# Optimization experiments

Measured on AMD Instinct MI355X. Metric: run time of the kernel, lower is better.

The kernel has to match this reference:

```python
import jax, jax.numpy as jnp
import numpy as np

EPS = 1e-5  # torch BatchNorm1d default eps
N_NODES, N_EDGES, F_IN, HID, N_LAYERS = 100000, 1600000, 128, 128, 3


def batchnorm(x):
    # affine=False, track_running_stats=False -> normalize with batch stats (biased var)
    m = x.mean(axis=0)
    v = x.var(axis=0)
    return (x - m) / jnp.sqrt(v + EPS)


def gcn_conv(x, W, b, src, dst, deg_inv_sqrt, n):
    # PyG GCNConv: add self-loops, symmetric norm D^-1/2 (A+I) D^-1/2, then linear.
    h = x @ W  # [N, H]
    norm = deg_inv_sqrt[src] * deg_inv_sqrt[dst]  # [E]
    agg = jax.ops.segment_sum(h[src] * norm[:, None], dst, num_segments=n)
    agg = agg + h * (deg_inv_sqrt ** 2)[:, None]  # self-loop term (norm = 1/deg_i)
    return agg + b


def setup_inputs() -> dict:
    key = jax.random.key(0)
    ks = jax.random.split(key, 12)
    x = jax.random.normal(ks[0], (N_NODES, F_IN), dtype=jnp.float32)
    edge_index = jax.random.randint(ks[1], (2, N_EDGES), 0, N_NODES, dtype=jnp.int32)
    s = 1.0 / np.sqrt(F_IN)
    W0 = jax.random.uniform(ks[2], (F_IN, HID), jnp.float32, -s, s)
    b0 = jax.random.uniform(ks[3], (HID,), jnp.float32, -s, s)
    sh = 1.0 / np.sqrt(HID)
    Ws = jax.random.uniform(ks[4], (N_LAYERS - 1, HID, HID), jnp.float32, -sh, sh)
    bs = jax.random.uniform(ks[5], (N_LAYERS - 1, HID), jnp.float32, -sh, sh)
    lin1_w = jax.random.uniform(ks[6], (HID, HID), jnp.float32, -sh, sh)
    lin1_b = jax.random.uniform(ks[7], (HID,), jnp.float32, -sh, sh)
    lin2_w = jax.random.uniform(ks[8], (HID, 2), jnp.float32, -sh, sh)
    lin2_b = jax.random.uniform(ks[9], (2,), jnp.float32, -sh, sh)
    return {"x": x, "edge_index": edge_index, "W0": W0, "b0": b0, "Ws": Ws,
            "bs": bs, "lin1_w": lin1_w, "lin1_b": lin1_b, "lin2_w": lin2_w, "lin2_b": lin2_b}


def reference(x, edge_index, W0, b0, Ws, bs, lin1_w, lin1_b, lin2_w, lin2_b):
    n = x.shape[0]
    src, dst = edge_index[0], edge_index[1]
    # degree with self-loops (computed on target nodes, as in PyG)
    deg = jax.ops.segment_sum(jnp.ones_like(dst, dtype=x.dtype), dst, num_segments=n) + 1.0
    deg_inv_sqrt = deg ** -0.5
    x = jax.nn.relu(batchnorm(gcn_conv(x, W0, b0, src, dst, deg_inv_sqrt, n)))
    for i in range(Ws.shape[0]):
        x = jax.nn.relu(batchnorm(gcn_conv(x, Ws[i], bs[i], src, dst, deg_inv_sqrt, n)))
    x = jax.nn.relu(batchnorm(x @ lin1_w + lin1_b))
    return x @ lin2_w + lin2_b
```

## Files before the change

kernel.cpp:

```cpp
#include <hip/hip_runtime.h>
#include <hip/hip_fp16.h>
#include <math.h>

#define HID 128
#define EPS 1e-5f
#define NBUCK 256
#define BCAP 10240
#define TILE 8192

typedef _Float16 half8 __attribute__((ext_vector_type(8)));
typedef _Float16 half4v __attribute__((ext_vector_type(4)));
typedef float f32x4 __attribute__((ext_vector_type(4)));

__global__ __launch_bounds__(256) void setup(float* __restrict__ psums,
                                             const float* __restrict__ W0,
                                             const float* __restrict__ Ws,
                                             const float* __restrict__ lin1w,
                                             _Float16* __restrict__ Wht,
                                             int* __restrict__ bcur,
                                             _Float16* __restrict__ zrow) {
    int g = blockIdx.x * 256 + threadIdx.x;
    if (g < 4 * 65536) psums[g] = 0.f;
    if (g < 65536) {
        int m = g >> 14;
        int idx = g & 16383;
        int n = idx >> 7, k = idx & 127;
        const float* W = (m == 0) ? W0 : (m == 1) ? Ws : (m == 2) ? (Ws + 16384) : lin1w;
        Wht[(size_t)m * 16384 + n * 128 + k] = (_Float16)W[k * 128 + n];
    }
    if (g < NBUCK) bcur[g] = 0;
    if (g < 128) zrow[g] = (_Float16)0.f;
}

__global__ __launch_bounds__(512) void bin_edges(const int* __restrict__ src, const int* __restrict__ dst,
                                                 int* __restrict__ bcur, int* __restrict__ pairPack, int E) {
    __shared__ int lpack[TILE];
    __shared__ unsigned char lbuck[TILE];
    __shared__ int hist[NBUCK], hscan[NBUCK], cur[NBUCK], delta[NBUCK];
    const int t = threadIdx.x;
    const int base = blockIdx.x * TILE;

    if (t < NBUCK) hist[t] = 0;
    __syncthreads();

    int pk[16], bk[16];
#pragma unroll
    for (int i = 0; i < 16; ++i) {
        int e = base + t + 512 * i;
        if (e < E) {
            int s = src[e], d = dst[e];
            pk[i] = (s << 9) | (d & 511);
            bk[i] = d >> 9;
            atomicAdd(&hist[bk[i]], 1);
        } else {
            bk[i] = -1;
        }
    }
    __syncthreads();

    int v = (t < NBUCK) ? hist[t] : 0;
    if (t < NBUCK) hscan[t] = v;
    __syncthreads();
    for (int off = 1; off < NBUCK; off <<= 1) {
        int u = (t >= off && t < NBUCK) ? hscan[t - off] : 0;
        __syncthreads();
        if (t < NBUCK) hscan[t] += u;
        __syncthreads();
    }
    if (t < NBUCK) cur[t] = hscan[t] - v;
    __syncthreads();

#pragma unroll
    for (int i = 0; i < 16; ++i) {
        if (bk[i] >= 0) {
            int p = atomicAdd(&cur[bk[i]], 1);
            lpack[p] = pk[i];
            lbuck[p] = (unsigned char)bk[i];
        }
    }
    __syncthreads();

    if (t < NBUCK) {
        int c = hist[t];
        if (c > 0) {
            int gbase = t * BCAP + atomicAdd(&bcur[t], c);
            delta[t] = gbase - (hscan[t] - c);
        }
    }
    __syncthreads();

    int total = hscan[NBUCK - 1];
    for (int i = t; i < total; i += 512) {
        int b = lbuck[i];
        pairPack[delta[b] + i] = lpack[i];
    }
}

__global__ __launch_bounds__(512) void bucket_csr(const int* __restrict__ pairPack,
                                                  const int* __restrict__ bcur,
                                                  int* __restrict__ cnt, float* __restrict__ dis,
                                                  int* __restrict__ rowptr,
                                                  int* __restrict__ srcsort, int N) {
    __shared__ int spair[BCAP];
    __shared__ int deg[512], sc[512], cur[512];
    const int b = blockIdx.x;
    const int t = threadIdx.x;
    deg[t] = 0;
    __syncthreads();
    int n = bcur[b];
    if (n > BCAP) n = BCAP;
    const int base = b * BCAP;
    for (int i = t; i < n; i += 512) {
        int p = pairPack[base + i];
        spair[i] = p;
        atomicAdd(&deg[p & 511], 1);
    }
    __syncthreads();
    int node = b * 512 + t;
    int d = deg[t];
    sc[t] = d;
    __syncthreads();
    for (int off = 1; off < 512; off <<= 1) {
        int u = (t >= off) ? sc[t - off] : 0;
        __syncthreads();
        sc[t] += u;
        __syncthreads();
    }
    int myoff = sc[t] - d;
    cur[t] = myoff;
    if (node < N) {
        cnt[node] = d;
        dis[node] = rsqrtf((float)d + 1.0f);
        rowptr[node] = base + myoff;
    }
    __syncthreads();
    for (int i = t; i < n; i += 512) {
        int p = spair[i];
        int pos = atomicAdd(&cur[p & 511], 1);
        srcsort[base + pos] = p >> 9;
    }
}

template <bool INF16, bool NORM, bool SCALEOUT, bool STATS>
__global__ __launch_bounds__(512) void gemm_mfma(const float* __restrict__ Xf,
                                                 const _Float16* __restrict__ Xh,
                                                 const _Float16* __restrict__ Wht,
                                                 const float* __restrict__ mean, const float* __restrict__ rstd,
                                                 const float* __restrict__ dis,
                                                 _Float16* __restrict__ Yh,
                                                 float* __restrict__ psum, float* __restrict__ psumsq,
                                                 int N) {
    __shared__ _Float16 sX[128 * 136];
    __shared__ _Float16 sW[128 * 136];
    __shared__ float gsum[STATS ? 8 : 1][128], gsq[STATS ? 8 : 1][128];
    const int tid = threadIdx.x;
    const int r0 = blockIdx.x * 128;

#pragma unroll
    for (int i = 0; i < 4; ++i) {
        int f = tid + 512 * i;
        int n = f >> 4;
        int k8 = (f & 15) * 8;
        *(half8*)&sW[n * 136 + k8] = *(const half8*)&Wht[n * 128 + k8];
    }

    if (INF16) {
#pragma unroll
        for (int i = 0; i < 4; ++i) {
            int f = tid + 512 * i;
            int rr = f >> 4;
            int c8 = (f & 15) * 8;
            int gr = r0 + rr;
            half8 hv = (half8)(_Float16)0.f;
            if (gr < N) hv = *(const half8*)&Xh[(size_t)gr * 128 + c8];
            if (NORM) {
#pragma unroll
                for (int e = 0; e < 8; ++e) {
                    float u = ((float)hv[e] - mean[c8 + e]) * rstd[c8 + e];
                    hv[e] = (_Float16)fmaxf(u, 0.f);
                }
            }
            *(half8*)&sX[rr * 136 + c8] = hv;
        }
    } else {
#pragma unroll
        for (int i = 0; i < 8; ++i) {
            int f = tid + 512 * i;
            int rr = f >> 5;
            int c4 = (f & 31) * 4;
            int gr = r0 + rr;
            float4 v = make_float4(0.f, 0.f, 0.f, 0.f);
            if (gr < N) v = *(const float4*)&Xf[(size_t)gr * 128 + c4];
            if (NORM) {
                float4 m4 = *(const float4*)&mean[c4];
                float4 s4 = *(const float4*)&rstd[c4];
                v.x = fmaxf((v.x - m4.x) * s4.x, 0.f);
                v.y = fmaxf((v.y - m4.y) * s4.y, 0.f);
                v.z = fmaxf((v.z - m4.z) * s4.z, 0.f);
                v.w = fmaxf((v.w - m4.w) * s4.w, 0.f);
            }
            half4v h;
            h.x = (_Float16)v.x; h.y = (_Float16)v.y; h.z = (_Float16)v.z; h.w = (_Float16)v.w;
            *(half4v*)&sX[rr * 136 + c4] = h;
        }
    }
    __syncthreads();

    const int wv = tid >> 6;
    const int lane = tid & 63;
    const int ln = lane & 15;
    const int quad = lane >> 4;

    half8 a[4];
    {
        const _Float16* sA = &sX[(wv * 16 + ln) * 136 + quad * 8];
#pragma unroll
        for (int kc = 0; kc < 4; ++kc) a[kc] = *(const half8*)&sA[kc * 32];
    }

    f32x4 acc[8];
#pragma unroll
    for (int ct = 0; ct < 8; ++ct) acc[ct] = (f32x4){0.f, 0.f, 0.f, 0.f};

    const _Float16* wbase = &sW[ln * 136 + quad * 8];
#pragma unroll
    for (int kc = 0; kc < 4; ++kc) {
#pragma unroll
        for (int ct = 0; ct < 8; ++ct) {
            half8 b = *(const half8*)&wbase[ct * 16 * 136 + kc * 32];
            acc[ct] = __builtin_amdgcn_mfma_f32_16x16x32_f16(a[kc], b, acc[ct], 0, 0, 0);
        }
    }

    float dv[4];
    int rr[4];
#pragma unroll
    for (int rg = 0; rg < 4; ++rg) {
        rr[rg] = r0 + wv * 16 + quad * 4 + rg;
        dv[rg] = (SCALEOUT && rr[rg] < N) ? dis[rr[rg]] : 1.f;
    }

    __syncthreads();
#pragma unroll
    for (int ct = 0; ct < 8; ++ct) {
        int col = ct * 16 + ln;
#pragma unroll
        for (int rg = 0; rg < 4; ++rg)
            sX[(wv * 16 + quad * 4 + rg) * 136 + col] = (_Float16)(acc[ct][rg] * dv[rg]);
    }
    __syncthreads();
#pragma unroll
    for (int i = 0; i < 4; ++i) {
        int f = tid + 512 * i;
        int rrr = f >> 4;
        int c8 = (f & 15) * 8;
        int gr = r0 + rrr;
        if (gr < N) *(half8*)&Yh[(size_t)gr * 128 + c8] = *(const half8*)&sX[rrr * 136 + c8];
    }

    if (STATS) {
#pragma unroll
        for (int ct = 0; ct < 8; ++ct) {
            float s = 0.f, s2 = 0.f;
#pragma unroll
            for (int rg = 0; rg < 4; ++rg) {
                if (rr[rg] < N) {
                    float v = acc[ct][rg];
                    s += v;
                    s2 += v * v;
                }
            }
            s += __shfl_xor(s, 16, 64);
            s += __shfl_xor(s, 32, 64);
            s2 += __shfl_xor(s2, 16, 64);
            s2 += __shfl_xor(s2, 32, 64);
            if (quad == 0) {
                gsum[wv][ct * 16 + ln] = s;
                gsq[wv][ct * 16 + ln] = s2;
            }
        }
        __syncthreads();
        int bkt = (blockIdx.x & 7) * 128;
        if (tid < 128) {
            float s = 0.f;
#pragma unroll
            for (int i = 0; i < 8; ++i) s += gsum[i][tid];
            atomicAdd(&psum[bkt + tid], s);
        } else if (tid < 256) {
            int c = tid - 128;
            float s2 = 0.f;
#pragma unroll
            for (int i = 0; i < 8; ++i) s2 += gsq[i][c];
            atomicAdd(&psumsq[bkt + c], s2);
        }
    }
}

__global__ __launch_bounds__(256) void aggregate_f16(const __half* __restrict__ hs,
                                                     const float* __restrict__ dis,
                                                     const int* __restrict__ rowptr,
                                                     const int* __restrict__ cnt,
                                                     const int* __restrict__ srcsort,
                                                     __half* __restrict__ outP,
                                                     float* __restrict__ psum, float* __restrict__ psumsq,
                                                     int N) {
    __shared__ float asum[4][128], asq[4][128];
    const int wv = threadIdx.x >> 6;
    const int lane = threadIdx.x & 63;
    const __half2* h2 = (const __half2*)hs;
    __half2* out2 = (__half2*)outP;
    const __half2 z = __float2half2_rn(0.f);

    float sx = 0.f, sy = 0.f, qx = 0.f, qy = 0.f;

#pragma unroll
    for (int rep = 0; rep < 4; ++rep) {
        const int node = __builtin_amdgcn_readfirstlane(blockIdx.x * 16 + wv * 4 + rep);

        __half2 acch[4];
        acch[0] = h2[(size_t)node * 64 + lane];
        acch[1] = z; acch[2] = z; acch[3] = z;

        const int beg = rowptr[node];
        const int end = beg + cnt[node];
        int e = beg;
        for (; e + 16 <= end; e += 16) {
            int s[16];
#pragma unroll
            for (int j = 0; j < 16; ++j) s[j] = srcsort[e + j];
            __half2 v[16];
#pragma unroll
            for (int j = 0; j < 16; ++j) v[j] = h2[(size_t)s[j] * 64 + lane];
#pragma unroll
            for (int j = 0; j < 16; ++j) acch[j & 3] = __hadd2(acch[j & 3], v[j]);
        }
        for (; e + 4 <= end; e += 4) {
            int s[4];
#pragma unroll
            for (int j = 0; j < 4; ++j) s[j] = srcsort[e + j];
            __half2 v[4];
#pragma unroll
            for (int j = 0; j < 4; ++j) v[j] = h2[(size_t)s[j] * 64 + lane];
#pragma unroll
            for (int j = 0; j < 4; ++j) acch[j & 3] = __hadd2(acch[j & 3], v[j]);
        }
        for (; e < end; ++e) {
            acch[0] = __hadd2(acch[0], h2[(size_t)srcsort[e] * 64 + lane]);
        }

        float2 f0 = __half22float2(acch[0]);
        float2 f1 = __half22float2(acch[1]);
        float2 f2 = __half22float2(acch[2]);
        float2 f3 = __half22float2(acch[3]);
        float di = dis[node];
        float rx = ((f0.x + f1.x) + (f2.x + f3.x)) * di;
        float ry = ((f0.y + f1.y) + (f2.y + f3.y)) * di;
        out2[(size_t)node * 64 + lane] = __floats2half2_rn(rx, ry);
        sx += rx; sy += ry;
        qx += rx * rx; qy += ry * ry;
    }

    asum[wv][2 * lane] = sx;
    asum[wv][2 * lane + 1] = sy;
    asq[wv][2 * lane] = qx;
    asq[wv][2 * lane + 1] = qy;
    __syncthreads();
    const int t = threadIdx.x;
    int bkt = (blockIdx.x & 255) * 128;
    if (t < 128) {
        float s = asum[0][t] + asum[1][t] + asum[2][t] + asum[3][t];
        atomicAdd(&psum[bkt + t], s);
    } else {
        int c = t - 128;
        float s2 = asq[0][c] + asq[1][c] + asq[2][c] + asq[3][c];
        atomicAdd(&psumsq[bkt + c], s2);
    }
}

__global__ __launch_bounds__(256) void finalize_stats_par(const float* __restrict__ psum,
                                                          const float* __restrict__ psumsq,
                                                          float* __restrict__ meanf, float* __restrict__ rstdf,
                                                          int N) {
    __shared__ float ls[256], ls2[256];
    int c = blockIdx.x;
    int t = threadIdx.x;
    ls[t] = psum[t * 128 + c];
    ls2[t] = psumsq[t * 128 + c];
    __syncthreads();
    for (int off = 128; off >= 1; off >>= 1) {
        if (t < off) { ls[t] += ls[t + off]; ls2[t] += ls2[t + off]; }
        __syncthreads();
    }
    if (t == 0) {
        float m = ls[0] / (float)N;
        float var = ls2[0] / (float)N - m * m;
        meanf[c] = m;
        rstdf[c] = rsqrtf(var + EPS);
    }
}

__global__ __launch_bounds__(256) void lin2_kernel(const __half* __restrict__ Q,
                                                   const float* __restrict__ psum,
                                                   const float* __restrict__ psumsq,
                                                   const float* __restrict__ W2,
                                                   const float* __restrict__ b2, float* __restrict__ out, int N) {
    __shared__ float sw0[128], sw1[128], sm[128], srs[128];
    int t = threadIdx.x;
    if (t < 128) {
        float s = 0.f, s2 = 0.f;
#pragma unroll
        for (int b = 0; b < 8; ++b) {
            s += psum[b * 128 + t];
            s2 += psumsq[b * 128 + t];
        }
        float m = s / (float)N;
        sm[t] = m;
        srs[t] = rsqrtf(s2 / (float)N - m * m + EPS);
        sw0[t] = W2[2 * t];
        sw1[t] = W2[2 * t + 1];
    }
    __syncthreads();
    int r = blockIdx.x * 256 + t;
    if (r >= N) return;
    const __half2* q2 = (const __half2*)Q;
    float acc0 = b2[0], acc1 = b2[1];
#pragma unroll 8
    for (int k2 = 0; k2 < 64; ++k2) {
        float2 f = __half22float2(q2[(size_t)r * 64 + k2]);
        int k = 2 * k2;
        float v0 = fmaxf((f.x - sm[k]) * srs[k], 0.f);
        float v1 = fmaxf((f.y - sm[k + 1]) * srs[k + 1], 0.f);
        acc0 += v0 * sw0[k] + v1 * sw0[k + 1];
        acc1 += v0 * sw1[k] + v1 * sw1[k + 1];
    }
    *(float2*)&out[2 * r] = make_float2(acc0, acc1);
}

extern "C" void kernel_launch(void* const* d_in, const int* in_sizes, int n_in,
                              void* d_out, int out_size, void* d_ws, size_t ws_size,
                              hipStream_t stream) {
    const float* x = (const float*)d_in[0];
    const int* ei = (const int*)d_in[1];
    const float* W0 = (const float*)d_in[2];
    const float* Ws = (const float*)d_in[4];
    const float* lin1w = (const float*)d_in[6];
    const float* lin2w = (const float*)d_in[8];
    const float* lin2b = (const float*)d_in[9];
    float* out = (float*)d_out;

    const int N = in_sizes[0] / HID;
    const int E = in_sizes[1] / 2;
    const int* src = ei;
    const int* dst = ei + E;

    char* w = (char*)d_ws;
    _Float16* Hs = (_Float16*)w;     w += ((size_t)N + 1) * HID * 2;
    _Float16* P16 = (_Float16*)w;    w += (size_t)N * HID * 2;
    float* dis = (float*)w;          w += (size_t)N * 4;
    int* cnt = (int*)w;              w += (size_t)N * 4;
    int* rowptr = (int*)w;           w += (size_t)N * 4;
    int* srcsort = (int*)w;          w += (size_t)NBUCK * BCAP * 4;
    float* psums = (float*)w;        w += 4 * 65536 * 4;
    float* meanf = (float*)w;        w += 128 * 4;
    float* rstdf = (float*)w;        w += 128 * 4;
    int* bcur = (int*)w;             w += NBUCK * 4;
    _Float16* Wht = (_Float16*)w;    w += 4 * 16384 * 2;

    int* pairPack = (int*)P16;

    const __half* HsH = (const __half*)Hs;
    __half* P16H = (__half*)P16;

    const int gGemm = (N + 127) / 128;
    const int gAgg = N / 16;
    const int nBuckUsed = (N + 511) / 512;
    const int gBin = (E + TILE - 1) / TILE;

    float* ps0 = psums;
    float* ps1 = psums + 65536;
    float* ps2 = psums + 2 * 65536;
    float* ps3 = psums + 3 * 65536;

    setup<<<1024, 256, 0, stream>>>(psums, W0, Ws, lin1w, Wht, bcur, Hs + (size_t)N * HID);
    bin_edges<<<gBin, 512, 0, stream>>>(src, dst, bcur, pairPack, E);
    bucket_csr<<<nBuckUsed, 512, 0, stream>>>(pairPack, bcur, cnt, dis, rowptr, srcsort, N);

    gemm_mfma<false, false, true, false><<<gGemm, 512, 0, stream>>>(
        x, nullptr, Wht, nullptr, nullptr, dis, Hs, nullptr, nullptr, N);
    aggregate_f16<<<gAgg, 256, 0, stream>>>(HsH, dis, rowptr, cnt, srcsort, P16H, ps0, ps0 + 32768, N);
    finalize_stats_par<<<128, 256, 0, stream>>>(ps0, ps0 + 32768, meanf, rstdf, N);

    for (int l = 0; l < 2; ++l) {
        const _Float16* Wl = Wht + (size_t)(1 + l) * 16384;
        float* psl = (l == 0) ? ps1 : ps2;
        gemm_mfma<true, true, true, false><<<gGemm, 512, 0, stream>>>(
            nullptr, P16, Wl, meanf, rstdf, dis, Hs, nullptr, nullptr, N);
        aggregate_f16<<<gAgg, 256, 0, stream>>>(HsH, dis, rowptr, cnt, srcsort, P16H, psl, psl + 32768, N);
        finalize_stats_par<<<128, 256, 0, stream>>>(psl, psl + 32768, meanf, rstdf, N);
    }

    gemm_mfma<true, true, false, true><<<gGemm, 512, 0, stream>>>(
        nullptr, P16, Wht + 3 * 16384, meanf, rstdf, nullptr, Hs, ps3, ps3 + 32768, N);

    lin2_kernel<<<(N + 255) / 256, 256, 0, stream>>>(HsH, ps3, ps3 + 32768, lin2w, lin2b, out, N);
}
```

Measured before the change: 404.4 us.

## Fuse BN stat finalization into GEMM prologue and shrink stat buckets

Removes the separate finalize_stats_par kernel after each aggregation. Each GEMM block now reduces 16 partial-sum buckets itself into shared mean/rstd before normalizing its input. Aggregation now writes its atomics into 16 buckets instead of 256, and each block covers 8 nodes instead of 16, which doubles the grid. This saves three launches and the memset of large partial buffers, at the cost of more atomic contention per bucket and a redundant small reduction in every GEMM block.

```diff
diff --git a/kernel.cpp b/kernel.cpp
--- a/kernel.cpp
+++ b/kernel.cpp
@@ -7,6 +7,7 @@
 #define NBUCK 256
 #define BCAP 10240
 #define TILE 8192
+#define SBUCK 16
 
 typedef _Float16 half8 __attribute__((ext_vector_type(8)));
 typedef _Float16 half4v __attribute__((ext_vector_type(4)));
@@ -20,7 +21,7 @@
                                              int* __restrict__ bcur,
                                              _Float16* __restrict__ zrow) {
     int g = blockIdx.x * 256 + threadIdx.x;
-    if (g < 4 * 65536) psums[g] = 0.f;
+    if (g < 4 * 2 * SBUCK * 128) psums[g] = 0.f;
     if (g < 65536) {
         int m = g >> 14;
         int idx = g & 16383;
@@ -145,7 +146,7 @@
 __global__ __launch_bounds__(512) void gemm_mfma(const float* __restrict__ Xf,
                                                  const _Float16* __restrict__ Xh,
                                                  const _Float16* __restrict__ Wht,
-                                                 const float* __restrict__ mean, const float* __restrict__ rstd,
+                                                 const float* __restrict__ psumIn, const float* __restrict__ psumsqIn,
                                                  const float* __restrict__ dis,
                                                  _Float16* __restrict__ Yh,
                                                  float* __restrict__ psum, float* __restrict__ psumsq,
@@ -153,8 +154,24 @@
     __shared__ _Float16 sX[128 * 136];
     __shared__ _Float16 sW[128 * 136];
     __shared__ float gsum[STATS ? 8 : 1][128], gsq[STATS ? 8 : 1][128];
+    __shared__ float sm[128], srs[128];
     const int tid = threadIdx.x;
     const int r0 = blockIdx.x * 128;
+
+    if (NORM) {
+        if (tid < 128) {
+            float s = 0.f, s2 = 0.f;
+#pragma unroll
+            for (int b = 0; b < SBUCK; ++b) {
+                s += psumIn[b * 128 + tid];
+                s2 += psumsqIn[b * 128 + tid];
+            }
+            float m = s / (float)N;
+            sm[tid] = m;
+            srs[tid] = rsqrtf(s2 / (float)N - m * m + EPS);
+        }
+        __syncthreads();
+    }
 
 #pragma unroll
     for (int i = 0; i < 4; ++i) {
@@ -176,7 +193,7 @@
             if (NORM) {
 #pragma unroll
                 for (int e = 0; e < 8; ++e) {
-                    float u = ((float)hv[e] - mean[c8 + e]) * rstd[c8 + e];
+                    float u = ((float)hv[e] - sm[c8 + e]) * srs[c8 + e];
                     hv[e] = (_Float16)fmaxf(u, 0.f);
                 }
             }
@@ -191,14 +208,6 @@
             int gr = r0 + rr;
             float4 v = make_float4(0.f, 0.f, 0.f, 0.f);
             if (gr < N) v = *(const float4*)&Xf[(size_t)gr * 128 + c4];
-            if (NORM) {
-                float4 m4 = *(const float4*)&mean[c4];
-                float4 s4 = *(const float4*)&rstd[c4];
-                v.x = fmaxf((v.x - m4.x) * s4.x, 0.f);
-                v.y = fmaxf((v.y - m4.y) * s4.y, 0.f);
-                v.z = fmaxf((v.z - m4.z) * s4.z, 0.f);
-                v.w = fmaxf((v.w - m4.w) * s4.w, 0.f);
-            }
             half4v h;
             h.x = (_Float16)v.x; h.y = (_Float16)v.y; h.z = (_Float16)v.z; h.w = (_Float16)v.w;
             *(half4v*)&sX[rr * 136 + c4] = h;
@@ -280,7 +289,7 @@
             }
         }
         __syncthreads();
-        int bkt = (blockIdx.x & 7) * 128;
+        int bkt = (blockIdx.x & (SBUCK - 1)) * 128;
         if (tid < 128) {
             float s = 0.f;
 #pragma unroll
@@ -314,8 +323,8 @@
     float sx = 0.f, sy = 0.f, qx = 0.f, qy = 0.f;
 
 #pragma unroll
-    for (int rep = 0; rep < 4; ++rep) {
-        const int node = __builtin_amdgcn_readfirstlane(blockIdx.x * 16 + wv * 4 + rep);
+    for (int rep = 0; rep < 2; ++rep) {
+        const int node = __builtin_amdgcn_readfirstlane(blockIdx.x * 8 + wv * 2 + rep);
 
         __half2 acch[4];
         acch[0] = h2[(size_t)node * 64 + lane];
@@ -366,7 +375,7 @@
     asq[wv][2 * lane + 1] = qy;
     __syncthreads();
     const int t = threadIdx.x;
-    int bkt = (blockIdx.x & 255) * 128;
+    int bkt = (blockIdx.x & (SBUCK - 1)) * 128;
     if (t < 128) {
         float s = asum[0][t] + asum[1][t] + asum[2][t] + asum[3][t];
         atomicAdd(&psum[bkt + t], s);
@@ -374,28 +383,6 @@
         int c = t - 128;
         float s2 = asq[0][c] + asq[1][c] + asq[2][c] + asq[3][c];
         atomicAdd(&psumsq[bkt + c], s2);
-    }
-}
-
-__global__ __launch_bounds__(256) void finalize_stats_par(const float* __restrict__ psum,
-                                                          const float* __restrict__ psumsq,
-                                                          float* __restrict__ meanf, float* __restrict__ rstdf,
-                                                          int N) {
-    __shared__ float ls[256], ls2[256];
-    int c = blockIdx.x;
-    int t = threadIdx.x;
-    ls[t] = psum[t * 128 + c];
-    ls2[t] = psumsq[t * 128 + c];
-    __syncthreads();
-    for (int off = 128; off >= 1; off >>= 1) {
-        if (t < off) { ls[t] += ls[t + off]; ls2[t] += ls2[t + off]; }
-        __syncthreads();
-    }
-    if (t == 0) {
-        float m = ls[0] / (float)N;
-        float var = ls2[0] / (float)N - m * m;
-        meanf[c] = m;
-        rstdf[c] = rsqrtf(var + EPS);
     }
 }
 
@@ -409,7 +396,7 @@
     if (t < 128) {
         float s = 0.f, s2 = 0.f;
 #pragma unroll
-        for (int b = 0; b < 8; ++b) {
+        for (int b = 0; b < SBUCK; ++b) {
             s += psum[b * 128 + t];
             s2 += psumsq[b * 128 + t];
         }
@@ -460,9 +447,7 @@
     int* cnt = (int*)w;              w += (size_t)N * 4;
     int* rowptr = (int*)w;           w += (size_t)N * 4;
     int* srcsort = (int*)w;          w += (size_t)NBUCK * BCAP * 4;
-    float* psums = (float*)w;        w += 4 * 65536 * 4;
-    float* meanf = (float*)w;        w += 128 * 4;
-    float* rstdf = (float*)w;        w += 128 * 4;
+    float* psums = (float*)w;        w += 4 * 2 * SBUCK * 128 * 4;
     int* bcur = (int*)w;             w += NBUCK * 4;
     _Float16* Wht = (_Float16*)w;    w += 4 * 16384 * 2;
 
@@ -472,14 +457,16 @@
     __half* P16H = (__half*)P16;
 
     const int gGemm = (N + 127) / 128;
-    const int gAgg = N / 16;
+    const int gAgg = N / 8;
     const int nBuckUsed = (N + 511) / 512;
     const int gBin = (E + TILE - 1) / TILE;
 
+    const int PSTR = 2 * SBUCK * 128;
     float* ps0 = psums;
-    float* ps1 = psums + 65536;
-    float* ps2 = psums + 2 * 65536;
-    float* ps3 = psums + 3 * 65536;
+    float* ps1 = psums + PSTR;
+    float* ps2 = psums + 2 * PSTR;
+    float* ps3 = psums + 3 * PSTR;
+    const int HALF = SBUCK * 128;
 
     setup<<<1024, 256, 0, stream>>>(psums, W0, Ws, lin1w, Wht, bcur, Hs + (size_t)N * HID);
     bin_edges<<<gBin, 512, 0, stream>>>(src, dst, bcur, pairPack, E);
@@ -487,20 +474,19 @@
 
     gemm_mfma<false, false, true, false><<<gGemm, 512, 0, stream>>>(
         x, nullptr, Wht, nullptr, nullptr, dis, Hs, nullptr, nullptr, N);
-    aggregate_f16<<<gAgg, 256, 0, stream>>>(HsH, dis, rowptr, cnt, srcsort, P16H, ps0, ps0 + 32768, N);
-    finalize_stats_par<<<128, 256, 0, stream>>>(ps0, ps0 + 32768, meanf, rstdf, N);
+    aggregate_f16<<<gAgg, 256, 0, stream>>>(HsH, dis, rowptr, cnt, srcsort, P16H, ps0, ps0 + HALF, N);
 
     for (int l = 0; l < 2; ++l) {
         const _Float16* Wl = Wht + (size_t)(1 + l) * 16384;
-        float* psl = (l == 0) ? ps1 : ps2;
+        float* psPrev = (l == 0) ? ps0 : ps1;
+        float* psCur = (l == 0) ? ps1 : ps2;
         gemm_mfma<true, true, true, false><<<gGemm, 512, 0, stream>>>(
-            nullptr, P16, Wl, meanf, rstdf, dis, Hs, nullptr, nullptr, N);
-        aggregate_f16<<<gAgg, 256, 0, stream>>>(HsH, dis, rowptr, cnt, srcsort, P16H, psl, psl + 32768, N);
-        finalize_stats_par<<<128, 256, 0, stream>>>(psl, psl + 32768, meanf, rstdf, N);
+            nullptr, P16, Wl, psPrev, psPrev + HALF, dis, Hs, nullptr, nullptr, N);
+        aggregate_f16<<<gAgg, 256, 0, stream>>>(HsH, dis, rowptr, cnt, srcsort, P16H, psCur, psCur + HALF, N);
     }
 
     gemm_mfma<true, true, false, true><<<gGemm, 512, 0, stream>>>(
-        nullptr, P16, Wht + 3 * 16384, meanf, rstdf, nullptr, Hs, ps3, ps3 + 32768, N);
-
-    lin2_kernel<<<(N + 255) / 256, 256, 0, stream>>>(HsH, ps3, ps3 + 32768, lin2w, lin2b, out, N);
-}
+        nullptr, P16, Wht + 3 * 16384, ps2, ps2 + HALF, nullptr, Hs, ps3, ps3 + HALF, N);
+
+    lin2_kernel<<<(N + 255) / 256, 256, 0, stream>>>(HsH, ps3, ps3 + HALF, lin2w, lin2b, out, N);
+}
```

Measured after the change: 408.4 us. No clear change (+1.0%).
